# Performance work log

Hardware: AMD Instinct MI355X
Metric: run time of the kernel (lower is better)

Reference implementation:

```python
import jax, jax.numpy as jnp
import numpy as np

D = 1024
E = 8
K = 2
NUM_ITER = 2
DT = 0.1
H = 64           # controller_hidden
CTX = 2 * D


def _gelu(t):
    return jax.nn.gelu(t, approximate=False)


def _inl(ctrl, x, v, mu):
    # ctrl: [T, 3D] -> alpha, beta, gate chunks of size D
    alpha_raw, beta_raw, gate_raw = jnp.split(ctrl, 3, axis=-1)
    alpha = jax.nn.sigmoid(alpha_raw)
    beta = jax.nn.softplus(beta_raw)
    gate = jax.nn.sigmoid(gate_raw)
    error = x - mu
    v_next = alpha * v - beta * error
    x_next = x + DT * gate * v_next
    return x_next, v_next


def setup_inputs() -> dict:
    key = jax.random.key(0)
    ks = jax.random.split(key, 20)
    s = 0.02
    inp = {
        'x': jax.random.normal(ks[0], (4, 4096, D), jnp.float32),
        # router MLP
        'w_r1': jax.random.normal(ks[1], (D, D // 4), jnp.float32) * s,
        'b_r1': jnp.zeros((D // 4,), jnp.float32),
        'w_r2': jax.random.normal(ks[2], (D // 4, E), jnp.float32) * s,
        'b_r2': jnp.zeros((E,), jnp.float32),
        # halt gate MLP
        'w_h1': jax.random.normal(ks[3], (D, D // 4), jnp.float32) * s,
        'b_h1': jnp.zeros((D // 4,), jnp.float32),
        'w_h2': jax.random.normal(ks[4], (D // 4, 1), jnp.float32) * s,
        'b_h2': jnp.zeros((1,), jnp.float32),
        # expert tables
        'expert_w1': jax.random.normal(ks[5], (E, CTX, H), jnp.float32) * s,
        'expert_b1': jnp.zeros((E, H), jnp.float32),
        'expert_w2': jax.random.normal(ks[6], (E, H, 3 * D), jnp.float32) * s,
        'expert_b2': jnp.zeros((E, 3 * D), jnp.float32),
        # shared expert
        'w_s1': jax.random.normal(ks[7], (CTX, H), jnp.float32) * s,
        'b_s1': jnp.zeros((H,), jnp.float32),
        'w_s2': jax.random.normal(ks[8], (H, 3 * D), jnp.float32) * s,
        'b_s2': jnp.zeros((3 * D,), jnp.float32),
        'shared_weight': jnp.asarray(0.5, jnp.float32),
        # refine MLP
        'w_f1': jax.random.normal(ks[9], (D, 2 * D), jnp.float32) * s,
        'b_f1': jnp.zeros((2 * D,), jnp.float32),
        'w_f2': jax.random.normal(ks[10], (2 * D, D), jnp.float32) * s,
        'b_f2': jnp.zeros((D,), jnp.float32),
        'integration_weight': jnp.full((D,), 0.5, jnp.float32),
        'mu': jnp.zeros((D,), jnp.float32),
    }
    return inp


def reference(x, w_r1, b_r1, w_r2, b_r2, w_h1, b_h1, w_h2, b_h2,
              expert_w1, expert_b1, expert_w2, expert_b2,
              w_s1, b_s1, w_s2, b_s2, shared_weight,
              w_f1, b_f1, w_f2, b_f2, integration_weight, mu):
    B, N, Dm = x.shape
    xf = x.reshape(B * N, Dm)                       # [T, D]

    # router: top-k over softmax probs, renormalized
    logits = _gelu(xf @ w_r1 + b_r1) @ w_r2 + b_r2  # [T, E]
    probs = jax.nn.softmax(logits, axis=-1)
    top_p, top_i = jax.lax.top_k(probs, K)          # [T, K]
    top_p = top_p / jnp.sum(top_p, axis=-1, keepdims=True)

    flat_idx = top_i.reshape(-1)                    # [T*K]
    flat_w = top_p.reshape(-1, 1)                   # [T*K, 1]

    v = jnp.zeros_like(xf)
    integrated = xf
    for _ in range(NUM_ITER):
        ctx = jnp.concatenate([integrated, v], axis=-1)     # [T, 2D]

        # shared expert path
        shared_ctrl = _gelu(ctx @ w_s1 + b_s1) @ w_s2 + b_s2
        x_shared, v_shared = _inl(shared_ctrl, integrated, v, mu)
        sw = jax.nn.sigmoid(shared_weight)

        # routed experts: gather per-token weights, per-token matvec
        ctx_e = jnp.repeat(ctx, K, axis=0)                  # [T*K, 2D]
        x_e = jnp.repeat(integrated, K, axis=0)
        v_e = jnp.repeat(v, K, axis=0)
        w1 = expert_w1[flat_idx]                            # [T*K, 2D, H]
        b1 = expert_b1[flat_idx]
        w2 = expert_w2[flat_idx]                            # [T*K, H, 3D]
        b2 = expert_b2[flat_idx]
        hidden = _gelu(jnp.einsum('tc,tch->th', ctx_e, w1) + b1)
        ctrl = jnp.einsum('th,tho->to', hidden, w2) + b2    # [T*K, 3D]
        x_r, v_r = _inl(ctrl, x_e, v_e, mu)
        x_r = (x_r * flat_w).reshape(B * N, K, Dm).sum(axis=1)
        v_r = (v_r * flat_w).reshape(B * N, K, Dm).sum(axis=1)

        x_next = sw * x_shared + (1.0 - sw) * x_r
        v_next = sw * v_shared + (1.0 - sw) * v_r

        halt = jax.nn.sigmoid(_gelu(x_next @ w_h1 + b_h1) @ w_h2 + b_h2)  # [T,1]
        refined = _gelu(x_next @ w_f1 + b_f1) @ w_f2 + b_f2               # [T,D]
        integrated = integrated + halt * refined * integration_weight
        v = v_next

    return integrated.reshape(B, N, Dm)
```

## Files before the change

### kernel.cpp

```cpp
#include <hip/hip_runtime.h>


#define TOK   16384
#define DDIM  1024
#define NEXP  8
#define DTC   0.1f
#define NDESC 320
#define GPAD  20480

using f32x4 = __attribute__((ext_vector_type(4))) float;
using bfv8  = __attribute__((ext_vector_type(8))) short;

__device__ __forceinline__ unsigned short f2bf(float x){
  unsigned u = __builtin_bit_cast(unsigned, x);
  u += 0x7fffu + ((u >> 16) & 1u);
  return (unsigned short)(u >> 16);
}
__device__ __forceinline__ float bf2f(unsigned short h){
  return __builtin_bit_cast(float, ((unsigned)h) << 16);
}
__device__ __forceinline__ float sigmf(float x){ return 1.0f/(1.0f+__expf(-x)); }
__device__ __forceinline__ float geluf(float x){
  float u = 1.595769122f * __builtin_fmaf(0.044715f*x*x, x, x);
  return x * sigmf(u);
}
__device__ __forceinline__ float softpf(float x){
  return fmaxf(x, 0.0f) + __logf(1.0f + __expf(-fabsf(x)));
}
__device__ __forceinline__ f32x4 mfma16(bfv8 a, bfv8 b, f32x4 c){
  return __builtin_amdgcn_mfma_f32_16x16x32_bf16(a, b, c, 0, 0, 0);
}
typedef __attribute__((address_space(1))) const void gvoid_t;
typedef __attribute__((address_space(3))) void svoid_t;
__device__ __forceinline__ void gload16(const void* g, void* l){
  __builtin_amdgcn_global_load_lds((gvoid_t*)g, (svoid_t*)l, 16, 0, 0);
}

__global__ __launch_bounds__(256) void transpose_cast(
    const float* __restrict__ src, unsigned short* __restrict__ dst, int R, int C)
{
  __shared__ float tile[32][33];
  size_t bo = (size_t)blockIdx.z * R * C;
  const float* s = src + bo;
  unsigned short* d = dst + bo;
  int c0 = blockIdx.x * 32, r0 = blockIdx.y * 32;
  int tx = threadIdx.x, ty = threadIdx.y;
  #pragma unroll
  for (int j = 0; j < 4; j++)
    tile[ty + 8*j][tx] = s[(size_t)(r0 + ty + 8*j) * C + c0 + tx];
  __syncthreads();
  #pragma unroll
  for (int j = 0; j < 4; j++)
    d[(size_t)(c0 + ty + 8*j) * R + r0 + tx] = f2bf(tile[tx][ty + 8*j]);
}

__global__ __launch_bounds__(256) void xinit_k(
    const float* __restrict__ xf, unsigned short* __restrict__ xb)
{
  const int n = TOK * 256;
  for (int i = blockIdx.x * 256 + threadIdx.x; i < n; i += gridDim.x * 256) {
    float4 f = ((const float4*)xf)[i];
    ushort4 u = {f2bf(f.x), f2bf(f.y), f2bf(f.z), f2bf(f.w)};
    ((ushort4*)xb)[i] = u;
  }
}

template<bool INIT>
__global__ __launch_bounds__(256) void ctxb_k(
    const float* __restrict__ xf, const int* __restrict__ tokmap,
    unsigned short* __restrict__ ctx)
{
  const int g = blockIdx.x, tid = threadIdx.x;
  const int t = tokmap[g];
  if (tid < 128) {
    uint4 o4 = {0,0,0,0};
    if (t >= 0) {
      const float4* s = (const float4*)(xf + (size_t)t * 1024) + tid * 2;
      float4 f0 = s[0], f1 = s[1];
      unsigned short tmp[8] = {f2bf(f0.x), f2bf(f0.y), f2bf(f0.z), f2bf(f0.w),
                               f2bf(f1.x), f2bf(f1.y), f2bf(f1.z), f2bf(f1.w)};
      o4 = *(uint4*)tmp;
    }
    *(uint4*)&ctx[(size_t)g * 2048 + tid * 8] = o4;
  } else if (INIT) {
    *(uint4*)&ctx[(size_t)g * 2048 + 1024 + (tid - 128) * 8] = uint4{0,0,0,0};
  }
}

template<int EPI>
__global__ __launch_bounds__(256) void gemm_k(
    const unsigned short* __restrict__ A, int lda,
    const unsigned short* __restrict__ BT,
    const float* __restrict__ bias, const float* __restrict__ bias2,
    int Kd, int N,
    unsigned short* __restrict__ obf, unsigned short* __restrict__ obf2,
    const float* __restrict__ halt, const float* __restrict__ iw,
    float* __restrict__ integ)
{
  __shared__ unsigned short As[128][64];
  __shared__ unsigned short Bs[128][64];
  const int total = gridDim.x * gridDim.y;
  const int bid = blockIdx.y * gridDim.x + blockIdx.x;
  const int swz = (bid & 7) * (total >> 3) + (bid >> 3);
  const int bx = swz % gridDim.x, by = swz / gridDim.x;

  const int tid  = threadIdx.x, lane = tid & 63, w = tid >> 6;
  const int wm   = w >> 1, wn = w & 1;
  const int gm0  = by * 128, gn0 = bx * 128;
  const int r8   = lane >> 3;
  const int sseg = (lane & 7) ^ r8;

  const unsigned short* aga[4];
  const unsigned short* bga[4];
  #pragma unroll
  for (int c = 0; c < 4; c++) {
    aga[c] = A  + (size_t)(gm0 + w*32 + c*8 + r8) * lda + sseg*8;
    bga[c] = BT + (size_t)(gn0 + w*32 + c*8 + r8) * Kd  + sseg*8;
  }

  f32x4 acc[4][4];
  #pragma unroll
  for (int i = 0; i < 4; i++)
    #pragma unroll
    for (int j = 0; j < 4; j++)
      acc[i][j] = f32x4{0.f,0.f,0.f,0.f};

  const int xr = (lane & 7) << 3;
  for (int k0 = 0; k0 < Kd; k0 += 64) {
    #pragma unroll
    for (int c = 0; c < 4; c++) gload16(aga[c] + k0, &As[w*32 + c*8][0]);
    #pragma unroll
    for (int c = 0; c < 4; c++) gload16(bga[c] + k0, &Bs[w*32 + c*8][0]);
    __syncthreads();
    #pragma unroll
    for (int kk = 0; kk < 64; kk += 32) {
      const int kof = kk + ((lane >> 4) << 3);
      bfv8 a[4], b[4];
      #pragma unroll
      for (int mf = 0; mf < 4; mf++)
        a[mf] = *(const bfv8*)&As[wm*64 + mf*16 + (lane & 15)][kof ^ xr];
      #pragma unroll
      for (int nf = 0; nf < 4; nf++)
        b[nf] = *(const bfv8*)&Bs[wn*64 + nf*16 + (lane & 15)][kof ^ xr];
      #pragma unroll
      for (int mf = 0; mf < 4; mf++)
        #pragma unroll
        for (int nf = 0; nf < 4; nf++)
          acc[mf][nf] = mfma16(a[mf], b[nf], acc[mf][nf]);
    }
    __syncthreads();
  }

  #pragma unroll
  for (int mf = 0; mf < 4; mf++) {
    #pragma unroll
    for (int nf = 0; nf < 4; nf++) {
      int col = gn0 + wn*64 + nf*16 + (lane & 15);
      float bc;
      if (EPI == 2) bc = (col < 2048) ? bias[col] : bias2[col - 2048];
      else          bc = bias[col];
      #pragma unroll
      for (int r = 0; r < 4; r++) {
        int row = gm0 + wm*64 + mf*16 + ((lane >> 4) << 2) + r;
        float v = acc[mf][nf][r] + bc;
        if (EPI == 0) {
          obf[(size_t)row * N + col] = f2bf(geluf(v));
        } else if (EPI == 2) {
          if (col < 2048) obf [(size_t)row * 2048 + col]         = f2bf(geluf(v));
          else            obf2[(size_t)row * 256 + (col - 2048)] = f2bf(geluf(v));
        } else {
          size_t ix = (size_t)row * DDIM + col;
          integ[ix] += halt[row] * v * iw[col];
        }
      }
    }
  }
}

__global__ __launch_bounds__(256) void router_k(
    const unsigned short* __restrict__ h1, const float* __restrict__ w_r2,
    const float* __restrict__ b_r2, int* __restrict__ topi, float* __restrict__ topw)
{
  int t = blockIdx.x * 4 + (threadIdx.x >> 6);
  int lane = threadIdx.x & 63;
  const unsigned short* hp = h1 + (size_t)t * 256 + lane * 4;
  float hv[4];
  #pragma unroll
  for (int j = 0; j < 4; j++) hv[j] = bf2f(hp[j]);
  float acc[8];
  #pragma unroll
  for (int e = 0; e < 8; e++) acc[e] = 0.f;
  #pragma unroll
  for (int j = 0; j < 4; j++) {
    const float* wr = w_r2 + (size_t)(lane*4 + j) * 8;
    #pragma unroll
    for (int e = 0; e < 8; e++) acc[e] += hv[j] * wr[e];
  }
  #pragma unroll
  for (int off = 32; off > 0; off >>= 1)
    #pragma unroll
    for (int e = 0; e < 8; e++) acc[e] += __shfl_xor(acc[e], off);
  if (lane == 0) {
    float lg[8];
    #pragma unroll
    for (int e = 0; e < 8; e++) lg[e] = acc[e] + b_r2[e];
    int i0 = 0; float m0 = lg[0];
    #pragma unroll
    for (int e = 1; e < 8; e++) if (lg[e] > m0) { m0 = lg[e]; i0 = e; }
    int i1 = -1; float m1 = -3.4e38f;
    #pragma unroll
    for (int e = 0; e < 8; e++) if (e != i0 && lg[e] > m1) { m1 = lg[e]; i1 = e; }
    float w0 = 1.0f / (1.0f + expf(m1 - m0));
    topi[t*2] = i0; topi[t*2+1] = i1;
    topw[t*2] = w0; topw[t*2+1] = 1.0f - w0;
  }
}

__global__ __launch_bounds__(256) void haltgate_k(
    const unsigned short* __restrict__ h1, const float* __restrict__ w_h2,
    const float* __restrict__ b_h2, float* __restrict__ halt)
{
  int t = blockIdx.x * 4 + (threadIdx.x >> 6);
  int lane = threadIdx.x & 63;
  const unsigned short* hp = h1 + (size_t)t * 256 + lane * 4;
  float s = 0.f;
  #pragma unroll
  for (int j = 0; j < 4; j++) s += bf2f(hp[j]) * w_h2[lane*4 + j];
  #pragma unroll
  for (int off = 32; off > 0; off >>= 1) s += __shfl_xor(s, off);
  if (lane == 0) halt[t] = sigmf(s + b_h2[0]);
}

__global__ __launch_bounds__(256) void pairb_k(
    const int* __restrict__ topi, const float* __restrict__ topw,
    int* __restrict__ cnt, int* __restrict__ plist, float* __restrict__ wA)
{
  int t = blockIdx.x * 256 + threadIdx.x;
  int a = topi[2*t], b = topi[2*t+1];
  float wa = topw[2*t];
  if (a > b) { int tmp = a; a = b; b = tmp; wa = 1.0f - wa; }
  int pid = a * 8 + b;
  int pos = atomicAdd(&cnt[pid], 1);
  plist[pid * TOK + pos] = t;
  wA[t] = wa;
}

__global__ void desc_k(const int* __restrict__ cnt, int4* __restrict__ desc,
                       int* __restrict__ ndesc, int* __restrict__ pbase)
{
  if (threadIdx.x == 0 && blockIdx.x == 0) {
    int nt = 0, rb = 0;
    for (int p = 0; p < 64; p++) {
      pbase[p] = rb;
      int c = cnt[p];
      for (int o = 0; o < c; o += 64) {
        int rem = c - o; if (rem > 64) rem = 64;
        desc[nt] = make_int4(p, rb + o, rem, 0);
        nt++;
      }
      rb += (c + 63) & ~63;
    }
    ndesc[0] = nt;
  }
}

__global__ __launch_bounds__(256) void pmap_k(
    const int* __restrict__ cnt, const int* __restrict__ pbase,
    const int* __restrict__ plist, int* __restrict__ tokmap)
{
  int pid = blockIdx.x;
  int pos = blockIdx.y * 256 + threadIdx.x;
  if (pos < cnt[pid]) {
    int t = plist[pid * TOK + pos];
    tokmap[pbase[pid] + pos] = t;
  }
}

__global__ __launch_bounds__(256) void exp1t_k(
    const unsigned short* __restrict__ ctx,
    const int4* __restrict__ desc, const int* __restrict__ ndesc,
    const unsigned short* __restrict__ ew1T, const float* __restrict__ eb1,
    const unsigned short* __restrict__ ws1T, const float* __restrict__ bs1,
    unsigned short* __restrict__ hiddenG)
{
  __shared__ unsigned short As[64][64];
  __shared__ unsigned short Bs[192][64];
  const int dx = blockIdx.x;
  if (dx >= ndesc[0]) return;
  int4 dd = desc[dx];
  const int pid = dd.x, rbt = dd.y;
  const int e0 = pid >> 3, e1 = pid & 7;
  const unsigned short* w1b[3] = { ew1T + (size_t)e0 * 64 * 2048,
                                   ew1T + (size_t)e1 * 64 * 2048, ws1T };
  const float* b1b[3] = { eb1 + e0 * 64, eb1 + e1 * 64, bs1 };
  const int tid = threadIdx.x, lane = tid & 63, w = tid >> 6;

  const int arow = w*8 + (lane >> 3);
  const int sseg = (lane & 7) ^ (lane >> 3);
  const unsigned short* asrc[2];
  #pragma unroll
  for (int q = 0; q < 2; q++)
    asrc[q] = ctx + (size_t)(rbt + q*32 + arow) * 2048 + sseg * 8;
  const unsigned short* bsrc[3][2];
  #pragma unroll
  for (int p = 0; p < 3; p++)
    #pragma unroll
    for (int q = 0; q < 2; q++)
      bsrc[p][q] = w1b[p] + (size_t)(q*32 + arow) * 2048 + sseg * 8;

  f32x4 acc[3][4];
  #pragma unroll
  for (int p = 0; p < 3; p++)
    #pragma unroll
    for (int j = 0; j < 4; j++)
      acc[p][j] = f32x4{0.f,0.f,0.f,0.f};

  const int xr = (lane & 7) << 3;
  for (int k0 = 0; k0 < 2048; k0 += 64) {
    #pragma unroll
    for (int q = 0; q < 2; q++) gload16(asrc[q] + k0, &As[q*32 + w*8][0]);
    #pragma unroll
    for (int p = 0; p < 3; p++)
      #pragma unroll
      for (int q = 0; q < 2; q++)
        gload16(bsrc[p][q] + k0, &Bs[p*64 + q*32 + w*8][0]);
    __syncthreads();
    #pragma unroll
    for (int kk = 0; kk < 64; kk += 32) {
      const int kof = kk + ((lane >> 4) << 3);
      bfv8 a = *(const bfv8*)&As[w*16 + (lane & 15)][kof ^ xr];
      #pragma unroll
      for (int p = 0; p < 3; p++)
        #pragma unroll
        for (int nf = 0; nf < 4; nf++) {
          bfv8 b = *(const bfv8*)&Bs[p*64 + nf*16 + (lane & 15)][kof ^ xr];
          acc[p][nf] = mfma16(a, b, acc[p][nf]);
        }
    }
    __syncthreads();
  }

  #pragma unroll
  for (int p = 0; p < 3; p++) {
    #pragma unroll
    for (int nf = 0; nf < 4; nf++) {
      int col = nf*16 + (lane & 15);
      float bb = b1b[p][col];
      #pragma unroll
      for (int r = 0; r < 4; r++) {
        int row = w*16 + ((lane >> 4) << 2) + r;
        hiddenG[(size_t)(3*rbt + p*64 + row) * 64 + col] =
            f2bf(geluf(acc[p][nf][r] + bb));
      }
    }
  }
}

__global__ __launch_bounds__(256) void exp2q_k(
    const unsigned short* __restrict__ hiddenG,
    const int4* __restrict__ desc, const int* __restrict__ ndesc,
    const int* __restrict__ tokmap, const float* __restrict__ wA,
    const unsigned short* __restrict__ ew2T, const float* __restrict__ eb2,
    const unsigned short* __restrict__ ws2T, const float* __restrict__ bs2,
    const float* __restrict__ swp, const float* __restrict__ mu,
    unsigned short* __restrict__ ctx, unsigned short* __restrict__ xaccB)
{
  __shared__ unsigned short Hs[192][64];
  __shared__ unsigned short W2s[192][64];
  __shared__ int   s_tok[64];
  __shared__ float s_w[64];
  const int dx = blockIdx.x, zq = blockIdx.y;
  if (dx >= ndesc[0]) return;
  int4 dd = desc[dx];
  const int pid = dd.x, rbt = dd.y, cnt = dd.z;
  const int e0 = pid >> 3, e1 = pid & 7;
  const int tid = threadIdx.x, lane = tid & 63, w = tid >> 6;
  const float sw = sigmf(swp[0]);

  if (tid < 64) {
    int t = tokmap[rbt + tid];
    if (t < 0) t = 0;
    s_tok[tid] = t; s_w[tid] = wA[t];
  }
  const int srow = w*8 + (lane >> 3);
  const int sseg = (lane & 7) ^ (lane >> 3);
  #pragma unroll
  for (int q = 0; q < 6; q++)
    gload16(hiddenG + (size_t)(3*rbt + q*32 + srow) * 64 + sseg*8,
            &Hs[q*32 + w*8][0]);
  __syncthreads();

  const unsigned short* w2b[3] = { ew2T + (size_t)e0*3072*64,
                                   ew2T + (size_t)e1*3072*64, ws2T };
  const float* b2b[3] = { eb2 + e0*3072, eb2 + e1*3072, bs2 };
  const int d0q = zq * 256;
  const int xr  = (lane & 7) << 3;
  const int cr4 = (lane >> 4) << 2;
  int toks[4]; float wa4[4];
  #pragma unroll
  for (int r = 0; r < 4; r++) {
    int row = w*16 + cr4 + r;
    toks[r] = s_tok[row]; wa4[r] = s_w[row];
  }

  for (int dcq = 0; dcq < 4; dcq++) {
    const int d00 = d0q + dcq*64;
    f32x4 A4[4], B4[4], C4[4], D4[4];
    #pragma unroll
    for (int cf = 0; cf < 4; cf++) {
      A4[cf] = f32x4{0.f,0.f,0.f,0.f}; B4[cf] = f32x4{0.f,0.f,0.f,0.f};
      C4[cf] = f32x4{0.f,0.f,0.f,0.f}; D4[cf] = f32x4{0.f,0.f,0.f,0.f};
    }
    #pragma unroll
    for (int path = 0; path < 3; path++) {
      #pragma unroll
      for (int q = 0; q < 6; q++) {
        int row  = q*32 + srow;
        int grow = (row >> 6)*1024 + d00 + (row & 63);
        gload16(w2b[path] + (size_t)grow*64 + sseg*8, &W2s[q*32 + w*8][0]);
      }
      __syncthreads();
      bfv8 a0 = *(const bfv8*)&Hs[path*64 + w*16 + (lane & 15)][(((lane>>4)<<3)) ^ xr];
      bfv8 a1 = *(const bfv8*)&Hs[path*64 + w*16 + (lane & 15)][(32 + ((lane>>4)<<3)) ^ xr];
      f32x4 acc[12];
      #pragma unroll
      for (int j = 0; j < 12; j++) acc[j] = f32x4{0.f,0.f,0.f,0.f};
      #pragma unroll
      for (int kk = 0; kk < 2; kk++) {
        const int kof = kk*32 + ((lane >> 4) << 3);
        #pragma unroll
        for (int nf = 0; nf < 12; nf++) {
          bfv8 b = *(const bfv8*)&W2s[nf*16 + (lane & 15)][kof ^ xr];
          acc[nf] = mfma16(kk == 0 ? a0 : a1, b, acc[nf]);
        }
      }
      const float* b2 = b2b[path];
      #pragma unroll
      for (int cf = 0; cf < 4; cf++) {
        int d = d00 + cf*16 + (lane & 15);
        float ba = b2[d], bb = b2[1024 + d], bg = b2[2048 + d];
        #pragma unroll
        for (int r = 0; r < 4; r++) {
          float cw = (path == 0) ? (1.f - sw) * wa4[r]
                   : (path == 1) ? (1.f - sw) * (1.f - wa4[r]) : sw;
          float al = sigmf(acc[cf][r] + ba);
          float be = softpf(acc[4 + cf][r] + bb);
          float ga = sigmf(acc[8 + cf][r] + bg);
          A4[cf][r] += cw * al;       B4[cf][r] += cw * be;
          C4[cf][r] += cw * ga * al;  D4[cf][r] += cw * ga * be;
        }
      }
      __syncthreads();
    }
    #pragma unroll
    for (int cf = 0; cf < 4; cf++) {
      int d = d00 + cf*16 + (lane & 15);
      float muv = mu[d];
      #pragma unroll
      for (int r = 0; r < 4; r++) {
        int row = w*16 + cr4 + r;
        size_t g = (size_t)(rbt + row);
        float xx = bf2f(ctx[g*2048 + d]);
        float vv = bf2f(ctx[g*2048 + 1024 + d]);
        float err = xx - muv;
        float vt = vv * A4[cf][r] - err * B4[cf][r];
        float gv = vv * C4[cf][r] - err * D4[cf][r];
        if (row < cnt) {
          xaccB[(size_t)toks[r]*1024 + d] = f2bf(xx + DTC * gv);
          ctx[g*2048 + 1024 + d]          = f2bf(vt);
        }
      }
    }
  }
}

extern "C" void kernel_launch(void* const* d_in, const int* in_sizes, int n_in,
                              void* d_out, int out_size, void* d_ws, size_t ws_size,
                              hipStream_t stream)
{
  const float* x    = (const float*)d_in[0];
  const float* w_r1 = (const float*)d_in[1];
  const float* b_r1 = (const float*)d_in[2];
  const float* w_r2 = (const float*)d_in[3];
  const float* b_r2 = (const float*)d_in[4];
  const float* w_h1 = (const float*)d_in[5];
  const float* b_h1 = (const float*)d_in[6];
  const float* w_h2 = (const float*)d_in[7];
  const float* b_h2 = (const float*)d_in[8];
  const float* ew1  = (const float*)d_in[9];
  const float* eb1  = (const float*)d_in[10];
  const float* ew2  = (const float*)d_in[11];
  const float* eb2  = (const float*)d_in[12];
  const float* w_s1 = (const float*)d_in[13];
  const float* b_s1 = (const float*)d_in[14];
  const float* w_s2 = (const float*)d_in[15];
  const float* b_s2 = (const float*)d_in[16];
  const float* swt  = (const float*)d_in[17];
  const float* w_f1 = (const float*)d_in[18];
  const float* b_f1 = (const float*)d_in[19];
  const float* w_f2 = (const float*)d_in[20];
  const float* b_f2 = (const float*)d_in[21];
  const float* iw   = (const float*)d_in[22];
  const float* mu   = (const float*)d_in[23];
  float* out = (float*)d_out;

  char* ws = (char*)d_ws;
  size_t off = 0;
  auto take = [&](size_t bytes) -> char* {
    char* p = ws + off;
    off = (off + bytes + 255) & ~(size_t)255;
    return p;
  };
  const size_t TD4 = (size_t)TOK * DDIM * 4;
  unsigned short* xaccB = (unsigned short*)take((size_t)TOK * 1024 * 2);
  unsigned short* ctx   = (unsigned short*)take((size_t)GPAD * 2048 * 2);
  unsigned short* rh    = (unsigned short*)take((size_t)TOK * 2048 * 2);
  unsigned short* hiddenG = (unsigned short*)take((size_t)3 * GPAD * 64 * 2);
  unsigned short* h1 = (unsigned short*)take((size_t)TOK * 256 * 2);
  float* halt = (float*)take((size_t)TOK * 4);
  int*   topi = (int*)take((size_t)TOK * 2 * 4);
  float* topw = (float*)take((size_t)TOK * 2 * 4);
  int*   cnt  = (int*)take(64 * 4);
  int*   ndsc = (int*)take(64);
  int*   pbase= (int*)take(64 * 4);
  int4*  desc = (int4*)take((size_t)NDESC * 16);
  int*   plist= (int*)take((size_t)64 * TOK * 4);
  float* wAa  = (float*)take((size_t)TOK * 4);
  int*   tokmap = (int*)take((size_t)GPAD * 4);
  unsigned short* w_r1T = (unsigned short*)take((size_t)256 * 1024 * 2);
  unsigned short* wFH   = (unsigned short*)take((size_t)2304 * 1024 * 2);
  unsigned short* w_f2T = (unsigned short*)take((size_t)1024 * 2048 * 2);
  unsigned short* w_s1T = (unsigned short*)take((size_t)64 * 2048 * 2);
  unsigned short* w_s2T = (unsigned short*)take((size_t)3072 * 64 * 2);
  unsigned short* ew1T  = (unsigned short*)take((size_t)NEXP * 64 * 2048 * 2);
  unsigned short* ew2T  = (unsigned short*)take((size_t)NEXP * 3072 * 64 * 2);
  if (off > ws_size) return;

  hipMemcpyAsync(out, x, TD4, hipMemcpyDeviceToDevice, stream);
  hipMemsetAsync(cnt, 0, 64 * 4, stream);
  hipMemsetAsync(tokmap, 0xFF, (size_t)GPAD * 4, stream);

  dim3 tb(32, 8);
  transpose_cast<<<dim3(  8, 32, 1), tb, 0, stream>>>(w_r1, w_r1T, 1024,  256);
  transpose_cast<<<dim3( 64, 32, 1), tb, 0, stream>>>(w_f1, wFH, 1024, 2048);
  transpose_cast<<<dim3(  8, 32, 1), tb, 0, stream>>>(w_h1, wFH + (size_t)2048*1024, 1024, 256);
  transpose_cast<<<dim3( 32, 64, 1), tb, 0, stream>>>(w_f2, w_f2T, 2048, 1024);
  transpose_cast<<<dim3(  2, 64, 1), tb, 0, stream>>>(w_s1, w_s1T, 2048,   64);
  transpose_cast<<<dim3( 96,  2, 1), tb, 0, stream>>>(w_s2, w_s2T,   64, 3072);
  transpose_cast<<<dim3(  2, 64, 8), tb, 0, stream>>>(ew1,  ew1T,  2048,   64);
  transpose_cast<<<dim3( 96,  2, 8), tb, 0, stream>>>(ew2,  ew2T,    64, 3072);

  xinit_k<<<2048, 256, 0, stream>>>(x, xaccB);
  gemm_k<0><<<dim3(2, 128), 256, 0, stream>>>(
      xaccB, 1024, w_r1T, b_r1, nullptr, 1024, 256, h1, nullptr,
      nullptr, nullptr, nullptr);
  router_k<<<TOK / 4, 256, 0, stream>>>(h1, w_r2, b_r2, topi, topw);
  pairb_k<<<TOK / 256, 256, 0, stream>>>(topi, topw, cnt, plist, wAa);
  desc_k<<<1, 64, 0, stream>>>(cnt, desc, ndsc, pbase);
  pmap_k<<<dim3(64, 64), 256, 0, stream>>>(cnt, pbase, plist, tokmap);
  ctxb_k<true><<<GPAD, 256, 0, stream>>>(out, tokmap, ctx);

  for (int it = 0; it < 2; it++) {
    exp1t_k<<<NDESC, 256, 0, stream>>>(ctx, desc, ndsc,
                                       ew1T, eb1, w_s1T, b_s1, hiddenG);
    exp2q_k<<<dim3(NDESC, 4), 256, 0, stream>>>(
        hiddenG, desc, ndsc, tokmap, wAa, ew2T, eb2, w_s2T, b_s2,
        swt, mu, ctx, xaccB);
    gemm_k<2><<<dim3(18, 128), 256, 0, stream>>>(
        xaccB, 1024, wFH, b_f1, b_h1, 1024, 2304, rh, h1,
        nullptr, nullptr, nullptr);
    haltgate_k<<<TOK / 4, 256, 0, stream>>>(h1, w_h2, b_h2, halt);
    gemm_k<1><<<dim3(8, 128), 256, 0, stream>>>(
        rh, 2048, w_f2T, b_f2, nullptr, 2048, 1024, nullptr, nullptr,
        halt, iw, out);
    if (it == 0)
      ctxb_k<false><<<GPAD, 256, 0, stream>>>(out, tokmap, ctx);
  }
}
```

Before: 1.382 ms.

## Double-buffer expert W2 tiles, keep hidden in registers, fuse ctx refresh into GEMM

The second expert kernel now loads its hidden activations straight into registers. It double-buffers the W2 weight tiles in shared memory, so the next tile's global load overlaps the current MFMA work, which removes one barrier per phase. The x and v context values are prefetched ahead of their epilogue use, and the grid is reordered so the four column quarters of one descriptor are scheduled next to each other. The separate ctxb pass between iterations is dropped: the refine GEMM epilogue now writes the bf16 context rows directly through a new token-to-slot map, at the cost of scattered writes and one more index array.

```diff
diff --git a/kernel.cpp b/kernel.cpp
--- a/kernel.cpp
+++ b/kernel.cpp
@@ -65,7 +65,6 @@
   }
 }
 
-template<bool INIT>
 __global__ __launch_bounds__(256) void ctxb_k(
     const float* __restrict__ xf, const int* __restrict__ tokmap,
     unsigned short* __restrict__ ctx)
@@ -82,7 +81,7 @@
       o4 = *(uint4*)tmp;
     }
     *(uint4*)&ctx[(size_t)g * 2048 + tid * 8] = o4;
-  } else if (INIT) {
+  } else {
     *(uint4*)&ctx[(size_t)g * 2048 + 1024 + (tid - 128) * 8] = uint4{0,0,0,0};
   }
 }
@@ -95,7 +94,8 @@
     int Kd, int N,
     unsigned short* __restrict__ obf, unsigned short* __restrict__ obf2,
     const float* __restrict__ halt, const float* __restrict__ iw,
-    float* __restrict__ integ)
+    float* __restrict__ integ, unsigned short* __restrict__ ctxX,
+    const int* __restrict__ pf)
 {
   __shared__ unsigned short As[128][64];
   __shared__ unsigned short Bs[128][64];
@@ -170,7 +170,9 @@
           else            obf2[(size_t)row * 256 + (col - 2048)] = f2bf(geluf(v));
         } else {
           size_t ix = (size_t)row * DDIM + col;
-          integ[ix] += halt[row] * v * iw[col];
+          float nv = integ[ix] + halt[row] * v * iw[col];
+          integ[ix] = nv;
+          if (ctxX) ctxX[(size_t)pf[row] * 2048 + col] = f2bf(nv);
         }
       }
     }
@@ -266,13 +268,15 @@
 
 __global__ __launch_bounds__(256) void pmap_k(
     const int* __restrict__ cnt, const int* __restrict__ pbase,
-    const int* __restrict__ plist, int* __restrict__ tokmap)
+    const int* __restrict__ plist, int* __restrict__ tokmap, int* __restrict__ pf)
 {
   int pid = blockIdx.x;
   int pos = blockIdx.y * 256 + threadIdx.x;
   if (pos < cnt[pid]) {
     int t = plist[pid * TOK + pos];
-    tokmap[pbase[pid] + pos] = t;
+    int g = pbase[pid] + pos;
+    tokmap[g] = t;
+    pf[t] = g;
   }
 }
 
@@ -356,7 +360,7 @@
   }
 }
 
-__global__ __launch_bounds__(256) void exp2q_k(
+__global__ __launch_bounds__(256) void exp2r_k(
     const unsigned short* __restrict__ hiddenG,
     const int4* __restrict__ desc, const int* __restrict__ ndesc,
     const int* __restrict__ tokmap, const float* __restrict__ wA,
@@ -365,11 +369,10 @@
     const float* __restrict__ swp, const float* __restrict__ mu,
     unsigned short* __restrict__ ctx, unsigned short* __restrict__ xaccB)
 {
-  __shared__ unsigned short Hs[192][64];
-  __shared__ unsigned short W2s[192][64];
+  __shared__ unsigned short W2s[2][192][64];
   __shared__ int   s_tok[64];
   __shared__ float s_w[64];
-  const int dx = blockIdx.x, zq = blockIdx.y;
+  const int zq = blockIdx.x, dx = blockIdx.y;
   if (dx >= ndesc[0]) return;
   int4 dd = desc[dx];
   const int pid = dd.x, rbt = dd.y, cnt = dd.z;
@@ -378,31 +381,45 @@
   const float sw = sigmf(swp[0]);
 
   if (tid < 64) {
-    int t = tokmap[rbt + tid];
-    if (t < 0) t = 0;
+    int t = tokmap[rbt + tid]; if (t < 0) t = 0;
     s_tok[tid] = t; s_w[tid] = wA[t];
   }
-  const int srow = w*8 + (lane >> 3);
-  const int sseg = (lane & 7) ^ (lane >> 3);
-  #pragma unroll
-  for (int q = 0; q < 6; q++)
-    gload16(hiddenG + (size_t)(3*rbt + q*32 + srow) * 64 + sseg*8,
-            &Hs[q*32 + w*8][0]);
-  __syncthreads();
 
   const unsigned short* w2b[3] = { ew2T + (size_t)e0*3072*64,
                                    ew2T + (size_t)e1*3072*64, ws2T };
   const float* b2b[3] = { eb2 + e0*3072, eb2 + e1*3072, bs2 };
-  const int d0q = zq * 256;
-  const int xr  = (lane & 7) << 3;
-  const int cr4 = (lane >> 4) << 2;
+  const int d0q  = zq * 256;
+  const int srow = w*8 + (lane >> 3);
+  const int sseg = (lane & 7) ^ (lane >> 3);
+  const int xr   = (lane & 7) << 3;
+  const int cr4  = (lane >> 4) << 2;
+  const int arow = w*16 + (lane & 15);
+  const int kof8 = (lane >> 4) << 3;
+
+  bfv8 afr[3][2];
+  #pragma unroll
+  for (int p = 0; p < 3; p++)
+    #pragma unroll
+    for (int kk = 0; kk < 2; kk++)
+      afr[p][kk] = *(const bfv8*)&hiddenG[
+          (size_t)(3*rbt + p*64 + arow) * 64 + kk*32 + kof8];
+
+  auto STAGE = [&](int b, int dcq, int path) {
+    const int d00 = d0q + dcq*64;
+    const unsigned short* w2 = w2b[path];
+    #pragma unroll
+    for (int q = 0; q < 6; q++) {
+      int row  = q*32 + srow;
+      int grow = (row >> 6)*1024 + d00 + (row & 63);
+      gload16(w2 + (size_t)grow*64 + sseg*8, &W2s[b][q*32 + w*8][0]);
+    }
+  };
+
+  STAGE(0, 0, 0);
   int toks[4]; float wa4[4];
-  #pragma unroll
-  for (int r = 0; r < 4; r++) {
-    int row = w*16 + cr4 + r;
-    toks[r] = s_tok[row]; wa4[r] = s_w[row];
-  }
-
+  float xx[4][4], vv[4][4];
+
+  #pragma unroll
   for (int dcq = 0; dcq < 4; dcq++) {
     const int d00 = d0q + dcq*64;
     f32x4 A4[4], B4[4], C4[4], D4[4];
@@ -413,25 +430,39 @@
     }
     #pragma unroll
     for (int path = 0; path < 3; path++) {
-      #pragma unroll
-      for (int q = 0; q < 6; q++) {
-        int row  = q*32 + srow;
-        int grow = (row >> 6)*1024 + d00 + (row & 63);
-        gload16(w2b[path] + (size_t)grow*64 + sseg*8, &W2s[q*32 + w*8][0]);
-      }
+      const int ph = dcq*3 + path;
       __syncthreads();
-      bfv8 a0 = *(const bfv8*)&Hs[path*64 + w*16 + (lane & 15)][(((lane>>4)<<3)) ^ xr];
-      bfv8 a1 = *(const bfv8*)&Hs[path*64 + w*16 + (lane & 15)][(32 + ((lane>>4)<<3)) ^ xr];
+      if (ph == 0) {
+        #pragma unroll
+        for (int r = 0; r < 4; r++) {
+          int row = w*16 + cr4 + r;
+          toks[r] = s_tok[row]; wa4[r] = s_w[row];
+        }
+        #pragma unroll
+        for (int cf = 0; cf < 4; cf++) {
+          int d = d00 + cf*16 + (lane & 15);
+          #pragma unroll
+          for (int r = 0; r < 4; r++) {
+            size_t g = (size_t)(rbt + w*16 + cr4 + r);
+            xx[cf][r] = bf2f(ctx[g*2048 + d]);
+            vv[cf][r] = bf2f(ctx[g*2048 + 1024 + d]);
+          }
+        }
+      }
+      if (ph < 11) {
+        const int phn = ph + 1;
+        STAGE(phn & 1, phn / 3, phn % 3);
+      }
       f32x4 acc[12];
       #pragma unroll
       for (int j = 0; j < 12; j++) acc[j] = f32x4{0.f,0.f,0.f,0.f};
       #pragma unroll
       for (int kk = 0; kk < 2; kk++) {
-        const int kof = kk*32 + ((lane >> 4) << 3);
+        const int kof = kk*32 + kof8;
         #pragma unroll
         for (int nf = 0; nf < 12; nf++) {
-          bfv8 b = *(const bfv8*)&W2s[nf*16 + (lane & 15)][kof ^ xr];
-          acc[nf] = mfma16(kk == 0 ? a0 : a1, b, acc[nf]);
+          bfv8 b = *(const bfv8*)&W2s[ph & 1][nf*16 + (lane & 15)][kof ^ xr];
+          acc[nf] = mfma16(afr[path][kk], b, acc[nf]);
         }
       }
       const float* b2 = b2b[path];
@@ -450,7 +481,6 @@
           C4[cf][r] += cw * ga * al;  D4[cf][r] += cw * ga * be;
         }
       }
-      __syncthreads();
     }
     #pragma unroll
     for (int cf = 0; cf < 4; cf++) {
@@ -460,14 +490,25 @@
       for (int r = 0; r < 4; r++) {
         int row = w*16 + cr4 + r;
         size_t g = (size_t)(rbt + row);
-        float xx = bf2f(ctx[g*2048 + d]);
-        float vv = bf2f(ctx[g*2048 + 1024 + d]);
-        float err = xx - muv;
-        float vt = vv * A4[cf][r] - err * B4[cf][r];
-        float gv = vv * C4[cf][r] - err * D4[cf][r];
+        float err = xx[cf][r] - muv;
+        float vt = vv[cf][r] * A4[cf][r] - err * B4[cf][r];
+        float gv = vv[cf][r] * C4[cf][r] - err * D4[cf][r];
         if (row < cnt) {
-          xaccB[(size_t)toks[r]*1024 + d] = f2bf(xx + DTC * gv);
+          xaccB[(size_t)toks[r]*1024 + d] = f2bf(xx[cf][r] + DTC * gv);
           ctx[g*2048 + 1024 + d]          = f2bf(vt);
+        }
+      }
+    }
+    if (dcq < 3) {
+      const int dn = d00 + 64;
+      #pragma unroll
+      for (int cf = 0; cf < 4; cf++) {
+        int d = dn + cf*16 + (lane & 15);
+        #pragma unroll
+        for (int r = 0; r < 4; r++) {
+          size_t g = (size_t)(rbt + w*16 + cr4 + r);
+          xx[cf][r] = bf2f(ctx[g*2048 + d]);
+          vv[cf][r] = bf2f(ctx[g*2048 + 1024 + d]);
         }
       }
     }
@@ -527,6 +568,7 @@
   int*   plist= (int*)take((size_t)64 * TOK * 4);
   float* wAa  = (float*)take((size_t)TOK * 4);
   int*   tokmap = (int*)take((size_t)GPAD * 4);
+  int*   pf     = (int*)take((size_t)TOK * 4);
   unsigned short* w_r1T = (unsigned short*)take((size_t)256 * 1024 * 2);
   unsigned short* wFH   = (unsigned short*)take((size_t)2304 * 1024 * 2);
   unsigned short* w_f2T = (unsigned short*)take((size_t)1024 * 2048 * 2);
@@ -553,27 +595,25 @@
   xinit_k<<<2048, 256, 0, stream>>>(x, xaccB);
   gemm_k<0><<<dim3(2, 128), 256, 0, stream>>>(
       xaccB, 1024, w_r1T, b_r1, nullptr, 1024, 256, h1, nullptr,
-      nullptr, nullptr, nullptr);
+      nullptr, nullptr, nullptr, nullptr, nullptr);
   router_k<<<TOK / 4, 256, 0, stream>>>(h1, w_r2, b_r2, topi, topw);
   pairb_k<<<TOK / 256, 256, 0, stream>>>(topi, topw, cnt, plist, wAa);
   desc_k<<<1, 64, 0, stream>>>(cnt, desc, ndsc, pbase);
-  pmap_k<<<dim3(64, 64), 256, 0, stream>>>(cnt, pbase, plist, tokmap);
-  ctxb_k<true><<<GPAD, 256, 0, stream>>>(out, tokmap, ctx);
+  pmap_k<<<dim3(64, 64), 256, 0, stream>>>(cnt, pbase, plist, tokmap, pf);
+  ctxb_k<<<GPAD, 256, 0, stream>>>(out, tokmap, ctx);
 
   for (int it = 0; it < 2; it++) {
     exp1t_k<<<NDESC, 256, 0, stream>>>(ctx, desc, ndsc,
                                        ew1T, eb1, w_s1T, b_s1, hiddenG);
-    exp2q_k<<<dim3(NDESC, 4), 256, 0, stream>>>(
+    exp2r_k<<<dim3(4, NDESC), 256, 0, stream>>>(
         hiddenG, desc, ndsc, tokmap, wAa, ew2T, eb2, w_s2T, b_s2,
         swt, mu, ctx, xaccB);
     gemm_k<2><<<dim3(18, 128), 256, 0, stream>>>(
         xaccB, 1024, wFH, b_f1, b_h1, 1024, 2304, rh, h1,
-        nullptr, nullptr, nullptr);
+        nullptr, nullptr, nullptr, nullptr, nullptr);
     haltgate_k<<<TOK / 4, 256, 0, stream>>>(h1, w_h2, b_h2, halt);
     gemm_k<1><<<dim3(8, 128), 256, 0, stream>>>(
         rh, 2048, w_f2T, b_f2, nullptr, 2048, 1024, nullptr, nullptr,
-        halt, iw, out);
-    if (it == 0)
-      ctxb_k<false><<<GPAD, 256, 0, stream>>>(out, tokmap, ctx);
-  }
-}
+        halt, iw, out, (it == 0) ? ctx : nullptr, pf);
+  }
+}
```

Result: faster. 1.324 ms (-4.2%).
